# Kernel optimization log

Hardware: AMD Instinct MI355X
Metric: run time of the kernel (lower is better)

Reference implementation:

```python
import jax, jax.numpy as jnp
import numpy as np

B, C, H, W = 64, 512, 32, 32
D = C // 8  # 64


def setup_inputs() -> dict:
    key = jax.random.key(0)
    k1, k2, k3, k4 = jax.random.split(key, 4)
    x = jax.random.normal(k1, (B, C, H, W), dtype=jnp.float32)
    query_m = jax.random.normal(k2, (H * W, D), dtype=jnp.float32)
    key_m = jax.random.normal(k3, (H * W, D), dtype=jnp.float32)
    # 1x1 conv C->C: weight [C_out, C_in], kaiming-ish scale
    value_w = jax.random.normal(k4, (C, C), dtype=jnp.float32) * (1.0 / np.sqrt(C))
    value_b = jnp.zeros((C,), dtype=jnp.float32)
    return {"x": x, "query_m": query_m, "key_m": key_m,
            "value_w": value_w, "value_b": value_b}


def reference(x, query_m, key_m, value_w, value_b):
    b, c, h, w = x.shape
    xf = x.reshape(b, c, h * w)                        # [B, C, N]
    q = jnp.einsum('bcn,nd->bcd', xf, query_m)         # [B, C, D]
    k = jnp.einsum('bcn,nd->bcd', xf, key_m)           # [B, C, D]
    energy = jnp.einsum('bcd,bed->bce', q, k)          # [B, C, C]
    energy = jax.nn.sigmoid(energy)
    attention = jax.nn.softmax(energy, axis=-2)        # softmax over rows (dim=-2)
    # 1x1 conv = channel matmul + bias
    v = jnp.einsum('bcn,oc->bon', xf, value_w) + value_b[None, :, None]  # [B, C, N]
    # out[b,j,n] = sum_i v[b,i,n] * attention[b,i,j]
    out = jnp.einsum('bin,bij->bjn', v, attention)     # [B, C, N]
    return out.reshape(b, c, h, w)
```

## Files before the change

### kernel.cpp

```cpp
#include <hip/hip_runtime.h>

#define BK 32

typedef __attribute__((ext_vector_type(8))) short bf16x8;
typedef __attribute__((ext_vector_type(4))) float f32x4;

__device__ __forceinline__ unsigned short f2bf(float f) {
  unsigned u = __builtin_bit_cast(unsigned, f);
  unsigned r = (u + 0x7FFFu + ((u >> 16) & 1u)) >> 16;
  return (unsigned short)r;
}
__device__ __forceinline__ float bf2f(unsigned short h) {
  return __builtin_bit_cast(float, (unsigned)h << 16);
}
__device__ __forceinline__ unsigned pack2(unsigned short a, unsigned short b) {
  return (unsigned)a | ((unsigned)b << 16);
}

__device__ __forceinline__ void gld_lds16(const void* g, void* l) {
  __builtin_amdgcn_global_load_lds(
      (const __attribute__((address_space(1))) unsigned int*)g,
      (__attribute__((address_space(3))) unsigned int*)l, 16, 0, 0);
}

#define SCHED0() __builtin_amdgcn_sched_barrier(0)
#define NTBAR() do { SCHED0(); __builtin_amdgcn_s_barrier(); SCHED0(); } while (0)
#define VMW(N) do { asm volatile("s_waitcnt vmcnt(" #N ")" ::: "memory"); SCHED0(); } while (0)

__device__ __forceinline__ void split8_store(float4 v0, float4 v1,
                                             unsigned short* Hdst,
                                             unsigned short* Ldst) {
  float f[8] = {v0.x, v0.y, v0.z, v0.w, v1.x, v1.y, v1.z, v1.w};
  unsigned short hh[8], ll[8];
#pragma unroll
  for (int i = 0; i < 8; ++i) {
    hh[i] = f2bf(f[i]);
    ll[i] = f2bf(f[i] - bf2f(hh[i]));
  }
  *reinterpret_cast<uint4*>(Hdst) = make_uint4(pack2(hh[0], hh[1]), pack2(hh[2], hh[3]),
                                               pack2(hh[4], hh[5]), pack2(hh[6], hh[7]));
  *reinterpret_cast<uint4*>(Ldst) = make_uint4(pack2(ll[0], ll[1]), pack2(ll[2], ll[3]),
                                               pack2(ll[4], ll[5]), pack2(ll[6], ll[7]));
}

__global__ __launch_bounds__(256) void qkm_split(const float* __restrict__ Qm,
                                                 const float* __restrict__ Km,
                                                 unsigned short* __restrict__ Th,
                                                 unsigned short* __restrict__ Tl) {
  __shared__ float lt[64][65];
  int k0 = blockIdx.x * 64;
  int half = blockIdx.y;
  const float* M = half ? Km : Qm;
  int t = threadIdx.x;
  int cl = (t & 15) * 4;
  int rl = t >> 4;
#pragma unroll
  for (int rr = 0; rr < 4; ++rr) {
    int r = rl + rr * 16;
    float4 v = *reinterpret_cast<const float4*>(&M[(long)(k0 + r) * 64 + cl]);
    lt[cl + 0][r] = v.x;
    lt[cl + 1][r] = v.y;
    lt[cl + 2][r] = v.z;
    lt[cl + 3][r] = v.w;
  }
  __syncthreads();
#pragma unroll
  for (int rr = 0; rr < 4; ++rr) {
    int c = rl + rr * 16;
    unsigned short h[4], lo[4];
#pragma unroll
    for (int i = 0; i < 4; ++i) {
      float f = lt[c][cl + i];
      h[i] = f2bf(f);
      lo[i] = f2bf(f - bf2f(h[i]));
    }
    *reinterpret_cast<uint2*>(&Th[(long)(half * 64 + c) * 1024 + k0 + cl]) =
        make_uint2(pack2(h[0], h[1]), pack2(h[2], h[3]));
    *reinterpret_cast<uint2*>(&Tl[(long)(half * 64 + c) * 1024 + k0 + cl]) =
        make_uint2(pack2(lo[0], lo[1]), pack2(lo[2], lo[3]));
  }
}

__global__ __launch_bounds__(256) void k1_mfma(const float* __restrict__ x,
                                               const unsigned short* __restrict__ Th,
                                               const unsigned short* __restrict__ Tl,
                                               float* __restrict__ qk) {
  __shared__ unsigned short Dh[2][128 * 32];
  __shared__ unsigned short Dl[2][128 * 32];
  __shared__ unsigned short Xh[2][64 * 32];
  __shared__ unsigned short Xl[2][64 * 32];
  const int t = threadIdx.x;
  const int l = t & 63;
  const int w = t >> 6;
  const int wr = w >> 1, wc = w & 1;
  const long mBase = (long)blockIdx.x * 64;

  f32x4 acc[4][2];
#pragma unroll
  for (int m = 0; m < 4; ++m)
#pragma unroll
    for (int n = 0; n < 2; ++n) acc[m][n] = (f32x4){0.f, 0.f, 0.f, 0.f};

  const int xrow_l = t >> 2;
  const int kslot = t & 3;
  const int xsl = kslot ^ ((t >> 3) & 3);
  const int srcslot = (l & 3) ^ ((l >> 3) & 3);
  const int frag_off = (l & 15) * 32 + ((((l >> 4) ^ (l >> 1)) & 3) * 8);
  const float* xrow = x + (mBase + xrow_l) * 1024;

#define K1_STAGE_B(k0, p)                                                     \
  {                                                                           \
    _Pragma("unroll") for (int c = 0; c < 2; ++c) {                           \
      int ch = c * 4 + w;                                                     \
      int row = ch * 16 + (l >> 2);                                           \
      gld_lds16(Th + (long)row * 1024 + (k0) + srcslot * 8, &Dh[p][ch * 512]);\
      gld_lds16(Tl + (long)row * 1024 + (k0) + srcslot * 8, &Dl[p][ch * 512]);\
    }                                                                         \
  }

#define K1_COMPUTE(p)                                                         \
  {                                                                           \
    bf16x8 dh[4], dl[4], xh[2], xl[2];                                        \
    _Pragma("unroll") for (int m = 0; m < 4; ++m) {                           \
      dh[m] = *reinterpret_cast<const bf16x8*>(&Dh[p][(wr * 64 + m * 16) * 32 + frag_off]); \
      dl[m] = *reinterpret_cast<const bf16x8*>(&Dl[p][(wr * 64 + m * 16) * 32 + frag_off]); \
    }                                                                         \
    _Pragma("unroll") for (int n = 0; n < 2; ++n) {                           \
      xh[n] = *reinterpret_cast<const bf16x8*>(&Xh[p][(wc * 32 + n * 16) * 32 + frag_off]); \
      xl[n] = *reinterpret_cast<const bf16x8*>(&Xl[p][(wc * 32 + n * 16) * 32 + frag_off]); \
    }                                                                         \
    _Pragma("unroll") for (int m = 0; m < 4; ++m)                             \
        _Pragma("unroll") for (int n = 0; n < 2; ++n) {                       \
      acc[m][n] = __builtin_amdgcn_mfma_f32_16x16x32_bf16(dh[m], xh[n], acc[m][n], 0, 0, 0); \
      acc[m][n] = __builtin_amdgcn_mfma_f32_16x16x32_bf16(dh[m], xl[n], acc[m][n], 0, 0, 0); \
      acc[m][n] = __builtin_amdgcn_mfma_f32_16x16x32_bf16(dl[m], xh[n], acc[m][n], 0, 0, 0); \
    }                                                                         \
  }

  {
    float4 p0 = *reinterpret_cast<const float4*>(&xrow[kslot * 8]);
    float4 p1 = *reinterpret_cast<const float4*>(&xrow[kslot * 8 + 4]);
    K1_STAGE_B(0, 0);
    split8_store(p0, p1, &Xh[0][xrow_l * 32 + xsl * 8], &Xl[0][xrow_l * 32 + xsl * 8]);
  }

  for (int k0 = 0; k0 < 1024; k0 += 64) {
    __syncthreads();
    float4 na0 = *reinterpret_cast<const float4*>(&xrow[k0 + 32 + kslot * 8]);
    float4 na1 = *reinterpret_cast<const float4*>(&xrow[k0 + 32 + kslot * 8 + 4]);
    K1_STAGE_B(k0 + 32, 1);
    K1_COMPUTE(0);
    split8_store(na0, na1, &Xh[1][xrow_l * 32 + xsl * 8], &Xl[1][xrow_l * 32 + xsl * 8]);
    __syncthreads();
    if (k0 + 64 < 1024) {
      float4 nb0 = *reinterpret_cast<const float4*>(&xrow[k0 + 64 + kslot * 8]);
      float4 nb1 = *reinterpret_cast<const float4*>(&xrow[k0 + 64 + kslot * 8 + 4]);
      K1_STAGE_B(k0 + 64, 0);
      K1_COMPUTE(1);
      split8_store(nb0, nb1, &Xh[0][xrow_l * 32 + xsl * 8], &Xl[0][xrow_l * 32 + xsl * 8]);
    } else {
      K1_COMPUTE(1);
    }
  }

#pragma unroll
  for (int m = 0; m < 4; ++m)
#pragma unroll
    for (int n = 0; n < 2; ++n) {
      int d0 = wr * 64 + m * 16 + (l >> 4) * 4;
      long xr = mBase + wc * 32 + n * 16 + (l & 15);
      *reinterpret_cast<float4*>(&qk[xr * 128 + d0]) =
          make_float4(acc[m][n][0], acc[m][n][1], acc[m][n][2], acc[m][n][3]);
    }
#undef K1_STAGE_B
#undef K1_COMPUTE
}

__global__ __launch_bounds__(256) void k2a_mfma(const float* __restrict__ qk,
                                                unsigned short* __restrict__ st) {
  __shared__ unsigned short Ah[128 * 64];
  __shared__ unsigned short Al[128 * 64];
  __shared__ unsigned short Bh[128 * 64];
  __shared__ unsigned short Bl[128 * 64];
  const int t = threadIdx.x;
  const int l = t & 63;
  const int w = t >> 6;
  const int wr = w >> 1, wc = w & 1;

  const int cpx = gridDim.x >> 3;
  const int orig = blockIdx.x;
  const int lw = (orig & 7) * cpx + (orig >> 3);
  const int b = lw >> 4;
  const int tile = lw & 15;
  const int iBase = (tile >> 2) * 128;
  const int jBase = (tile & 3) * 128;
  const float* qb = qk + (long)b * 512 * 128;

  {
    const int r = t >> 1;
    const int kh = t & 1;
    const float* qa = &qb[(long)(iBase + r) * 128 + kh * 32];
    const float* kb = &qb[(long)(jBase + r) * 128 + 64 + kh * 32];
#pragma unroll
    for (int c = 0; c < 4; ++c) {
      int s = (kh * 4 + c) ^ (r & 7);
      float4 a0 = *reinterpret_cast<const float4*>(&qa[c * 8]);
      float4 a1 = *reinterpret_cast<const float4*>(&qa[c * 8 + 4]);
      split8_store(a0, a1, &Ah[r * 64 + s * 8], &Al[r * 64 + s * 8]);
      float4 b0 = *reinterpret_cast<const float4*>(&kb[c * 8]);
      float4 b1 = *reinterpret_cast<const float4*>(&kb[c * 8 + 4]);
      split8_store(b0, b1, &Bh[r * 64 + s * 8], &Bl[r * 64 + s * 8]);
    }
  }
  __syncthreads();

  f32x4 acc[4][4];
#pragma unroll
  for (int m = 0; m < 4; ++m)
#pragma unroll
    for (int n = 0; n < 4; ++n) acc[m][n] = (f32x4){0.f, 0.f, 0.f, 0.f};

#pragma unroll
  for (int ks = 0; ks < 2; ++ks) {
    bf16x8 ah[4], al4[4], bh[4], bl4[4];
#pragma unroll
    for (int m = 0; m < 4; ++m) {
      int row = wr * 64 + m * 16 + (l & 15);
      int off = row * 64 + ((ks * 4 + (l >> 4)) ^ (row & 7)) * 8;
      ah[m] = *reinterpret_cast<const bf16x8*>(&Ah[off]);
      al4[m] = *reinterpret_cast<const bf16x8*>(&Al[off]);
    }
#pragma unroll
    for (int n = 0; n < 4; ++n) {
      int row = wc * 64 + n * 16 + (l & 15);
      int off = row * 64 + ((ks * 4 + (l >> 4)) ^ (row & 7)) * 8;
      bh[n] = *reinterpret_cast<const bf16x8*>(&Bh[off]);
      bl4[n] = *reinterpret_cast<const bf16x8*>(&Bl[off]);
    }
#pragma unroll
    for (int m = 0; m < 4; ++m)
#pragma unroll
      for (int n = 0; n < 4; ++n) {
        acc[m][n] = __builtin_amdgcn_mfma_f32_16x16x32_bf16(ah[m], bh[n], acc[m][n], 0, 0, 0);
        acc[m][n] = __builtin_amdgcn_mfma_f32_16x16x32_bf16(ah[m], bl4[n], acc[m][n], 0, 0, 0);
        acc[m][n] = __builtin_amdgcn_mfma_f32_16x16x32_bf16(al4[m], bh[n], acc[m][n], 0, 0, 0);
      }
  }

  unsigned short* sb = st + (long)b * 512 * 512;
#pragma unroll
  for (int m = 0; m < 4; ++m)
#pragma unroll
    for (int n = 0; n < 4; ++n) {
      int i0 = iBase + wr * 64 + m * 16 + (l >> 4) * 4;
      int j = jBase + wc * 64 + n * 16 + (l & 15);
      unsigned short p[4];
#pragma unroll
      for (int reg = 0; reg < 4; ++reg) {
        float sg = 1.0f / (1.0f + __expf(-acc[m][n][reg]));
        p[reg] = f2bf(__expf(sg));
      }
      *reinterpret_cast<uint2*>(&sb[(long)j * 512 + i0]) = *reinterpret_cast<uint2*>(p);
    }
}

__global__ __launch_bounds__(256) void k2b_rsum(const unsigned short* __restrict__ st,
                                                const float* __restrict__ bias,
                                                float* __restrict__ rsum,
                                                float* __restrict__ attbias) {
  int jg = blockIdx.x * 4 + (threadIdx.x >> 6);
  int l = threadIdx.x & 63;
  const unsigned short* row = st + (long)jg * 512 + l * 8;
  ushort4 u0 = *reinterpret_cast<const ushort4*>(row);
  ushort4 u1 = *reinterpret_cast<const ushort4*>(row + 4);
  float4 b0 = *reinterpret_cast<const float4*>(&bias[l * 8]);
  float4 b1 = *reinterpret_cast<const float4*>(&bias[l * 8 + 4]);
  float f0 = bf2f(u0.x), f1 = bf2f(u0.y), f2 = bf2f(u0.z), f3 = bf2f(u0.w);
  float f4 = bf2f(u1.x), f5 = bf2f(u1.y), f6 = bf2f(u1.z), f7 = bf2f(u1.w);
  float sum = (f0 + f1) + (f2 + f3) + ((f4 + f5) + (f6 + f7));
  float sumb = f0 * b0.x + f1 * b0.y + f2 * b0.z + f3 * b0.w +
               f4 * b1.x + f5 * b1.y + f6 * b1.z + f7 * b1.w;
#pragma unroll
  for (int off = 32; off > 0; off >>= 1) {
    sum += __shfl_down(sum, off);
    sumb += __shfl_down(sumb, off);
  }
  if (l == 0) {
    float r = 1.0f / sum;
    rsum[jg] = r;
    attbias[jg] = sumb * r;
  }
}

__global__ __launch_bounds__(256) void transpose_conv(const float* __restrict__ in,
                                                      unsigned short* __restrict__ out,
                                                      int inRows, int inCols,
                                                      long inBatch, long outBatch) {
  __shared__ unsigned short lt[64][65];
  int b = blockIdx.z;
  int r0 = blockIdx.y * 64;
  int c0 = blockIdx.x * 64;
  const float* I = in + (long)b * inBatch;
  unsigned short* O = out + (long)b * outBatch;
  int t = threadIdx.x;
  int cl = (t & 15) * 4;
  int rl = t >> 4;
#pragma unroll
  for (int rr = 0; rr < 4; ++rr) {
    int r = rl + rr * 16;
    float4 v = *reinterpret_cast<const float4*>(&I[(long)(r0 + r) * inCols + c0 + cl]);
    lt[cl + 0][r] = f2bf(v.x);
    lt[cl + 1][r] = f2bf(v.y);
    lt[cl + 2][r] = f2bf(v.z);
    lt[cl + 3][r] = f2bf(v.w);
  }
  __syncthreads();
#pragma unroll
  for (int rr = 0; rr < 4; ++rr) {
    int c = rl + rr * 16;
    unsigned short v[4] = {lt[c][cl], lt[c][cl + 1], lt[c][cl + 2], lt[c][cl + 3]};
    *reinterpret_cast<uint2*>(&O[(long)(c0 + c) * inRows + r0 + cl]) =
        *reinterpret_cast<uint2*>(&v[0]);
  }
}

template <int MODE>
__global__ __launch_bounds__(512) void mfma_nt256(const unsigned short* __restrict__ Abase,
                                                  const unsigned short* __restrict__ Bbase,
                                                  const float* __restrict__ rowscale,
                                                  unsigned short* __restrict__ Wout,
                                                  float* __restrict__ Fout) {
  __shared__ unsigned short As[2][256 * 64];
  __shared__ unsigned short Bs[2][256 * 64];
  const int t = threadIdx.x;
  const int l = t & 63;
  const int w = t >> 6;
  const int wr = w >> 2;
  const int wc = w & 3;

  const int cpx = gridDim.x >> 3;
  const int orig = blockIdx.x;
  const int lw = (orig & 7) * cpx + (orig >> 3);
  const int TPB_SH = (MODE == 0) ? 2 : 3;
  const int b = lw >> TPB_SH;
  const int tile = lw & ((1 << TPB_SH) - 1);
  const int mBase = (tile >> 1) * 256;
  const int nBase = (tile & 1) * 256;

  const unsigned short* Ag = Abase + ((MODE == 0) ? 0L : (long)b * (1024 * 512)) + (long)mBase * 512;
  const unsigned short* Bg = Bbase + (long)b * (512 * 512) + (long)nBase * 512;

  f32x4 acc[8][4];
#pragma unroll
  for (int m = 0; m < 8; ++m)
#pragma unroll
    for (int n = 0; n < 4; ++n) acc[m][n] = (f32x4){0.f, 0.f, 0.f, 0.f};

  const int srcslot = (l & 7) ^ (l >> 3);

#define NT_STAGE(kt, p)                                                        \
  {                                                                            \
    _Pragma("unroll") for (int pr = 0; pr < 4; ++pr) {                         \
      int rr = pr * 64 + w * 8 + (l >> 3);                                     \
      gld_lds16(Ag + (long)rr * 512 + (kt) * 64 + srcslot * 8,                 \
                &As[p][(pr * 64 + w * 8) * 64]);                               \
      gld_lds16(Bg + (long)rr * 512 + (kt) * 64 + srcslot * 8,                 \
                &Bs[p][(pr * 64 + w * 8) * 64]);                               \
    }                                                                          \
  }

#define NT_COMPUTE(p)                                                          \
  {                                                                            \
    _Pragma("unroll") for (int kk = 0; kk < 2; ++kk) {                         \
      const int so = ((kk * 4 + (l >> 4)) ^ (l & 7)) * 8;                      \
      bf16x8 af[8], bfr[4];                                                    \
      _Pragma("unroll") for (int m = 0; m < 8; ++m)                            \
        af[m] = *reinterpret_cast<const bf16x8*>(                              \
            &As[p][(wr * 128 + m * 16 + (l & 15)) * 64 + so]);                 \
      _Pragma("unroll") for (int n = 0; n < 4; ++n)                            \
        bfr[n] = *reinterpret_cast<const bf16x8*>(                             \
            &Bs[p][(wc * 64 + n * 16 + (l & 15)) * 64 + so]);                  \
      _Pragma("unroll") for (int m = 0; m < 8; ++m)                            \
        _Pragma("unroll") for (int n = 0; n < 4; ++n)                          \
          acc[m][n] = __builtin_amdgcn_mfma_f32_16x16x32_bf16(af[m], bfr[n],   \
                                                              acc[m][n], 0, 0, 0); \
    }                                                                          \
  }

  NT_STAGE(0, 0);
  NT_STAGE(1, 1);
  VMW(8);
  NTBAR();

  for (int kt = 0; kt < 8; ++kt) {
    const int p = kt & 1;
    __builtin_amdgcn_s_setprio(1);
    NT_COMPUTE(p);
    __builtin_amdgcn_s_setprio(0);
    NTBAR();
    if (kt < 6) {
      NT_STAGE(kt + 2, p);
      VMW(8);
    } else {
      VMW(0);
    }
    NTBAR();
  }
#undef NT_STAGE
#undef NT_COMPUTE

  if (MODE == 0) {
    unsigned short* W = Wout + (long)b * (512 * 512);
#pragma unroll
    for (int n = 0; n < 4; ++n) {
      int j = nBase + wc * 64 + n * 16 + (l & 15);
      float rs = rowscale[b * 512 + j];
#pragma unroll
      for (int m = 0; m < 8; ++m) {
        int c0 = mBase + wr * 128 + m * 16 + (l >> 4) * 4;
        unsigned short p[4];
#pragma unroll
        for (int reg = 0; reg < 4; ++reg) p[reg] = f2bf(acc[m][n][reg] * rs);
        *reinterpret_cast<uint2*>(&W[(long)j * 512 + c0]) = *reinterpret_cast<uint2*>(p);
      }
    }
  } else {
    float* O = Fout + (long)b * (512 * 1024);
#pragma unroll
    for (int n = 0; n < 4; ++n) {
      int j = nBase + wc * 64 + n * 16 + (l & 15);
      float ab = rowscale[b * 512 + j];
#pragma unroll
      for (int m = 0; m < 8; ++m) {
        int n0 = mBase + wr * 128 + m * 16 + (l >> 4) * 4;
        *reinterpret_cast<float4*>(&O[(long)j * 1024 + n0]) =
            make_float4(acc[m][n][0] + ab, acc[m][n][1] + ab,
                        acc[m][n][2] + ab, acc[m][n][3] + ab);
      }
    }
  }
}

extern "C" void kernel_launch(void* const* d_in, const int* in_sizes, int n_in,
                              void* d_out, int out_size, void* d_ws, size_t ws_size,
                              hipStream_t stream) {
  const float* x  = (const float*)d_in[0];
  const float* Qm = (const float*)d_in[1];
  const float* Km = (const float*)d_in[2];
  const float* vw = (const float*)d_in[3];
  const float* vb = (const float*)d_in[4];
  float* out = (float*)d_out;

  float* ws = (float*)d_ws;
  float* qk = ws;
  unsigned short* st   = (unsigned short*)(ws + 4194304);
  unsigned short* weff = (unsigned short*)(ws + 4194304 + 8388608);
  unsigned short* xbT  = (unsigned short*)(ws + 4194304 + 16777216);
  unsigned short* vwT  = (unsigned short*)(ws + 4194304 + 33554432);
  unsigned short* qkTh = (unsigned short*)(ws + 4194304 + 33554432 + 131072);
  unsigned short* qkTl = qkTh + 131072;
  float* rsum    = ws + 4194304 + 33554432 + 131072 + 131072;
  float* attbias = rsum + 32768;

  transpose_conv<<<dim3(16, 8, 64), 256, 0, stream>>>(x, xbT, 512, 1024, 524288L, 524288L);
  transpose_conv<<<dim3(8, 8, 1), 256, 0, stream>>>(vw, vwT, 512, 512, 0L, 0L);
  qkm_split<<<dim3(16, 2), 256, 0, stream>>>(Qm, Km, qkTh, qkTl);
  k1_mfma<<<512, 256, 0, stream>>>(x, qkTh, qkTl, qk);
  k2a_mfma<<<1024, 256, 0, stream>>>(qk, st);
  k2b_rsum<<<8192, 256, 0, stream>>>(st, vb, rsum, attbias);
  mfma_nt256<0><<<256, 512, 0, stream>>>(vwT, st, rsum, weff, nullptr);
  mfma_nt256<1><<<512, 512, 0, stream>>>(xbT, weff, attbias, nullptr, out);
}
```

Baseline: 221.4 us.

## Interleave async LDS staging with MFMA phases in NT GEMM pipeline

Replaces the compute-all-then-stage-all loop of the NT GEMM with eight fine-grained phases per iteration. Each phase reads a slice of A fragments from LDS, issues two global-to-LDS loads for upcoming tiles, synchronises, and runs a small batch of MFMAs, with vmcnt waits placed partway through. The goal is to overlap global loads with matrix math and cut the long barrier stalls. The risk is correctness of the buffer reuse ordering, since parts of a buffer are overwritten while other rows are still being read, plus the cost of more barriers. The tail iterations reload tile 7 redundantly.

```diff
diff --git a/kernel.cpp b/kernel.cpp
--- a/kernel.cpp
+++ b/kernel.cpp
@@ -26,6 +26,8 @@
 #define SCHED0() __builtin_amdgcn_sched_barrier(0)
 #define NTBAR() do { SCHED0(); __builtin_amdgcn_s_barrier(); SCHED0(); } while (0)
 #define VMW(N) do { asm volatile("s_waitcnt vmcnt(" #N ")" ::: "memory"); SCHED0(); } while (0)
+#define LGKM0() do { asm volatile("s_waitcnt lgkmcnt(0)" ::: "memory"); SCHED0(); } while (0)
+#define MFMA16(a, b, c) __builtin_amdgcn_mfma_f32_16x16x32_bf16(a, b, c, 0, 0, 0)
 
 __device__ __forceinline__ void split8_store(float4 v0, float4 v1,
                                              unsigned short* Hdst,
@@ -131,9 +133,9 @@
     }                                                                         \
     _Pragma("unroll") for (int m = 0; m < 4; ++m)                             \
         _Pragma("unroll") for (int n = 0; n < 2; ++n) {                       \
-      acc[m][n] = __builtin_amdgcn_mfma_f32_16x16x32_bf16(dh[m], xh[n], acc[m][n], 0, 0, 0); \
-      acc[m][n] = __builtin_amdgcn_mfma_f32_16x16x32_bf16(dh[m], xl[n], acc[m][n], 0, 0, 0); \
-      acc[m][n] = __builtin_amdgcn_mfma_f32_16x16x32_bf16(dl[m], xh[n], acc[m][n], 0, 0, 0); \
+      acc[m][n] = MFMA16(dh[m], xh[n], acc[m][n]);                            \
+      acc[m][n] = MFMA16(dh[m], xl[n], acc[m][n]);                            \
+      acc[m][n] = MFMA16(dl[m], xh[n], acc[m][n]);                            \
     }                                                                         \
   }
 
@@ -241,9 +243,9 @@
     for (int m = 0; m < 4; ++m)
 #pragma unroll
       for (int n = 0; n < 4; ++n) {
-        acc[m][n] = __builtin_amdgcn_mfma_f32_16x16x32_bf16(ah[m], bh[n], acc[m][n], 0, 0, 0);
-        acc[m][n] = __builtin_amdgcn_mfma_f32_16x16x32_bf16(ah[m], bl4[n], acc[m][n], 0, 0, 0);
-        acc[m][n] = __builtin_amdgcn_mfma_f32_16x16x32_bf16(al4[m], bh[n], acc[m][n], 0, 0, 0);
+        acc[m][n] = MFMA16(ah[m], bh[n], acc[m][n]);
+        acc[m][n] = MFMA16(ah[m], bl4[n], acc[m][n]);
+        acc[m][n] = MFMA16(al4[m], bh[n], acc[m][n]);
       }
   }
 
@@ -357,57 +359,75 @@
     for (int n = 0; n < 4; ++n) acc[m][n] = (f32x4){0.f, 0.f, 0.f, 0.f};
 
   const int srcslot = (l & 7) ^ (l >> 3);
-
-#define NT_STAGE(kt, p)                                                        \
+  const int so0 = ((l >> 4) ^ (l & 7)) * 8;
+  const int so1 = ((4 + (l >> 4)) ^ (l & 7)) * 8;
+
+#define STG_A(p, tt, pr)                                                       \
+  gld_lds16(Ag + (long)((pr) * 64 + w * 8 + (l >> 3)) * 512 + (tt) * 64 + srcslot * 8, \
+            &As[p][((pr) * 64 + w * 8) * 64]);
+#define STG_B(p, tt, pr)                                                       \
+  gld_lds16(Bg + (long)((pr) * 64 + w * 8 + (l >> 3)) * 512 + (tt) * 64 + srcslot * 8, \
+            &Bs[p][((pr) * 64 + w * 8) * 64]);
+
+#define PHASE(p, q, STAGE_STMT, VMSTMT)                                        \
   {                                                                            \
-    _Pragma("unroll") for (int pr = 0; pr < 4; ++pr) {                         \
-      int rr = pr * 64 + w * 8 + (l >> 3);                                     \
-      gld_lds16(Ag + (long)rr * 512 + (kt) * 64 + srcslot * 8,                 \
-                &As[p][(pr * 64 + w * 8) * 64]);                               \
-      gld_lds16(Bg + (long)rr * 512 + (kt) * 64 + srcslot * 8,                 \
-                &Bs[p][(pr * 64 + w * 8) * 64]);                               \
+    bf16x8 a00 = *reinterpret_cast<const bf16x8*>(                             \
+        &As[p][(wr * 128 + (2 * (q)) * 16 + (l & 15)) * 64 + so0]);            \
+    bf16x8 a01 = *reinterpret_cast<const bf16x8*>(                             \
+        &As[p][(wr * 128 + (2 * (q)) * 16 + (l & 15)) * 64 + so1]);            \
+    bf16x8 a10 = *reinterpret_cast<const bf16x8*>(                             \
+        &As[p][(wr * 128 + (2 * (q) + 1) * 16 + (l & 15)) * 64 + so0]);        \
+    bf16x8 a11 = *reinterpret_cast<const bf16x8*>(                             \
+        &As[p][(wr * 128 + (2 * (q) + 1) * 16 + (l & 15)) * 64 + so1]);        \
+    if ((q) == 0) {                                                            \
+      _Pragma("unroll") for (int n = 0; n < 4; ++n) {                          \
+        bfr0[n] = *reinterpret_cast<const bf16x8*>(                            \
+            &Bs[p][(wc * 64 + n * 16 + (l & 15)) * 64 + so0]);                 \
+        bfr1[n] = *reinterpret_cast<const bf16x8*>(                            \
+            &Bs[p][(wc * 64 + n * 16 + (l & 15)) * 64 + so1]);                 \
+      }                                                                        \
     }                                                                          \
-  }
-
-#define NT_COMPUTE(p)                                                          \
-  {                                                                            \
-    _Pragma("unroll") for (int kk = 0; kk < 2; ++kk) {                         \
-      const int so = ((kk * 4 + (l >> 4)) ^ (l & 7)) * 8;                      \
-      bf16x8 af[8], bfr[4];                                                    \
-      _Pragma("unroll") for (int m = 0; m < 8; ++m)                            \
-        af[m] = *reinterpret_cast<const bf16x8*>(                              \
-            &As[p][(wr * 128 + m * 16 + (l & 15)) * 64 + so]);                 \
-      _Pragma("unroll") for (int n = 0; n < 4; ++n)                            \
-        bfr[n] = *reinterpret_cast<const bf16x8*>(                             \
-            &Bs[p][(wc * 64 + n * 16 + (l & 15)) * 64 + so]);                  \
-      _Pragma("unroll") for (int m = 0; m < 8; ++m)                            \
-        _Pragma("unroll") for (int n = 0; n < 4; ++n)                          \
-          acc[m][n] = __builtin_amdgcn_mfma_f32_16x16x32_bf16(af[m], bfr[n],   \
-                                                              acc[m][n], 0, 0, 0); \
+    STAGE_STMT;                                                                \
+    SCHED0();                                                                  \
+    __builtin_amdgcn_s_barrier();                                              \
+    LGKM0();                                                                   \
+    __builtin_amdgcn_s_setprio(1);                                             \
+    _Pragma("unroll") for (int n = 0; n < 4; ++n) {                            \
+      acc[2 * (q)][n] = MFMA16(a00, bfr0[n], acc[2 * (q)][n]);                 \
+      acc[2 * (q)][n] = MFMA16(a01, bfr1[n], acc[2 * (q)][n]);                 \
+      acc[2 * (q) + 1][n] = MFMA16(a10, bfr0[n], acc[2 * (q) + 1][n]);         \
+      acc[2 * (q) + 1][n] = MFMA16(a11, bfr1[n], acc[2 * (q) + 1][n]);         \
     }                                                                          \
-  }
-
-  NT_STAGE(0, 0);
-  NT_STAGE(1, 1);
-  VMW(8);
+    __builtin_amdgcn_s_setprio(0);                                             \
+    VMSTMT;                                                                    \
+    NTBAR();                                                                   \
+  }
+
+  bf16x8 bfr0[4], bfr1[4];
+
+  STG_A(0, 0, 0); STG_A(0, 0, 1); STG_A(0, 0, 2); STG_A(0, 0, 3);
+  STG_B(0, 0, 0); STG_B(0, 0, 1); STG_B(0, 0, 2); STG_B(0, 0, 3);
+  STG_B(1, 1, 0); STG_B(1, 1, 1); STG_B(1, 1, 2); STG_B(1, 1, 3);
+  STG_A(1, 1, 0); STG_A(1, 1, 2);
+  VMW(6);
   NTBAR();
 
-  for (int kt = 0; kt < 8; ++kt) {
-    const int p = kt & 1;
-    __builtin_amdgcn_s_setprio(1);
-    NT_COMPUTE(p);
-    __builtin_amdgcn_s_setprio(0);
-    NTBAR();
-    if (kt < 6) {
-      NT_STAGE(kt + 2, p);
-      VMW(8);
-    } else {
-      VMW(0);
-    }
-    NTBAR();
-  }
-#undef NT_STAGE
-#undef NT_COMPUTE
+  for (int it = 0; it < 4; ++it) {
+    const int t1 = 2 * it + 1;
+    const int t2 = (2 * it + 2 < 8) ? 2 * it + 2 : 7;
+    const int t3 = (2 * it + 3 < 8) ? 2 * it + 3 : 7;
+    PHASE(0, 0, { STG_A(1, t1, 1); STG_A(1, t1, 3); }, );
+    PHASE(0, 1, { STG_B(0, t2, 0); STG_B(0, t2, 1); }, VMW(10));
+    PHASE(0, 2, { STG_B(0, t2, 2); STG_B(0, t2, 3); }, );
+    PHASE(0, 3, { STG_A(0, t2, 0); STG_A(0, t2, 2); }, VMW(8));
+    PHASE(1, 0, { STG_A(0, t2, 1); STG_A(0, t2, 3); }, );
+    PHASE(1, 1, { STG_B(1, t3, 0); STG_B(1, t3, 1); }, VMW(10));
+    PHASE(1, 2, { STG_B(1, t3, 2); STG_B(1, t3, 3); }, );
+    PHASE(1, 3, { STG_A(1, t3, 0); STG_A(1, t3, 2); }, VMW(8));
+  }
+#undef PHASE
+#undef STG_A
+#undef STG_B
 
   if (MODE == 0) {
     unsigned short* W = Wout + (long)b * (512 * 512);
```

Result: faster. 212.7 us (-3.9%).
